# Kernel optimization log

Hardware: AMD Instinct MI355X
Metric: run time of the kernel (lower is better)

Reference implementation:

```python
import jax, jax.numpy as jnp
import numpy as np

HID = 512      # hidden_dim
MID = 256      # hid_dim
COND_D = 256   # condition_op_dim
OP_D = 32      # operator_len
EX_D = 32      # extra_info_num
L, N, T = 16, 1024, 8
EPS = 1e-5


def _lstm_cell(x_proj, h, c, Whh, bhh):
    # x_proj: precomputed x @ Wih.T + bih, shape [B, 4H]
    gates = x_proj + h @ Whh.T + bhh
    i, f, g, o = jnp.split(gates, 4, axis=-1)
    i = jax.nn.sigmoid(i); f = jax.nn.sigmoid(f)
    g = jnp.tanh(g); o = jax.nn.sigmoid(o)
    c = f * c + i * g
    h = o * jnp.tanh(c)
    return h, c


def _batchnorm(x, gamma, beta):
    mu = x.mean(0)
    var = x.var(0)  # biased, matches PyTorch training-mode normalization
    return gamma * (x - mu) * jax.lax.rsqrt(var + EPS) + beta


def setup_inputs() -> dict:
    key = jax.random.key(0)
    ks = jax.random.split(key, 24)
    s = lambda *sh: 0.05
    inp = {
        'operators': jax.random.normal(ks[0], (L, N, OP_D), jnp.float32),
        'extra_infos': jax.random.normal(ks[1], (L, N, EX_D), jnp.float32),
        'conditions': jax.random.normal(ks[2], (L, N, T, COND_D), jnp.float32),
        'condition_masks': jnp.ones((L, N, 1), jnp.float32),
        'mapping': jax.random.randint(ks[3], (L, N, 2), 0, N + 1, jnp.int32).astype(jnp.int64),
        'lstm1_Wih': jax.random.normal(ks[4], (4 * HID, COND_D), jnp.float32) * 0.05,
        'lstm1_Whh': jax.random.normal(ks[5], (4 * HID, HID), jnp.float32) * 0.05,
        'lstm1_bih': jnp.zeros((4 * HID,), jnp.float32),
        'lstm1_bhh': jnp.zeros((4 * HID,), jnp.float32),
        'cond_W': jax.random.normal(ks[6], (MID, HID), jnp.float32) * 0.05,
        'cond_b': jnp.zeros((MID,), jnp.float32),
        'bn1_g': jnp.ones((MID,), jnp.float32),
        'bn1_b': jnp.zeros((MID,), jnp.float32),
        'lstm2_Wih': jax.random.normal(ks[7], (4 * HID, OP_D + EX_D + MID), jnp.float32) * 0.05,
        'lstm2_Whh': jax.random.normal(ks[8], (4 * HID, HID), jnp.float32) * 0.05,
        'lstm2_bih': jnp.zeros((4 * HID,), jnp.float32),
        'lstm2_bhh': jnp.zeros((4 * HID,), jnp.float32),
        'bn2_g': jnp.ones((HID,), jnp.float32),
        'bn2_b': jnp.zeros((HID,), jnp.float32),
    }
    return inp


def reference(operators, extra_infos, conditions, condition_masks, mapping,
              lstm1_Wih, lstm1_Whh, lstm1_bih, lstm1_bhh,
              cond_W, cond_b, bn1_g, bn1_b,
              lstm2_Wih, lstm2_Whh, lstm2_bih, lstm2_bhh,
              bn2_g, bn2_b):
    B = L * N
    x = conditions.reshape(B, T, COND_D)
    # lstm1 over conditions; precompute input projections for all steps
    xp = jnp.einsum('btd,gd->btg', x, lstm1_Wih) + lstm1_bih  # [B,T,4H]

    def step1(carry, xt):
        h, c = carry
        h, c = _lstm_cell(xt, h, c, lstm1_Whh, lstm1_bhh)
        return (h, c), None

    h0 = jnp.zeros((B, HID), xp.dtype)
    (h1, _), _ = jax.lax.scan(step1, (h0, h0), jnp.swapaxes(xp, 0, 1))

    last = jax.nn.relu(h1 @ cond_W.T + cond_b)       # [B, MID]
    last = _batchnorm(last, bn1_g, bn1_b).reshape(L, N, MID)

    out = jnp.concatenate([operators, extra_infos, last], axis=2)  # [L,N,IN2]
    xp2 = jnp.einsum('lnd,gd->lng', out, lstm2_Wih) + lstm2_bih    # [L,N,4H]

    hz = jnp.zeros((N, HID), xp2.dtype)
    h, c = _lstm_cell(xp2[L - 1], hz, hz, lstm2_Whh, lstm2_bhh)

    mapping = mapping.astype(jnp.int32)
    levels = jnp.arange(L - 2, -1, -1)

    def tree_step(carry, idx):
        h, c = carry
        mp = mapping[idx]  # [N,2]
        pad = jnp.zeros((1, HID), h.dtype)
        ph = jnp.concatenate([pad, h], 0)  # [N+1,H]
        pc = jnp.concatenate([pad, c], 0)
        h = (ph[mp[:, 0]] + ph[mp[:, 1]]) * 0.5
        c = (pc[mp[:, 0]] + pc[mp[:, 1]]) * 0.5
        h, c = _lstm_cell(xp2[idx], h, c, lstm2_Whh, lstm2_bhh)
        return (h, c), None

    (h, c), _ = jax.lax.scan(tree_step, (h, c), levels)

    # batch_size == N since all operator rows are nonzero
    return _batchnorm(h, bn2_g, bn2_b)  # [N, HID]
```

## Files before the change

kernel.cpp:

```cpp
#include <hip/hip_runtime.h>
#include <hip/hip_bf16.h>
#include <stdint.h>


typedef __bf16 bf16;
typedef __bf16 bf16x8 __attribute__((ext_vector_type(8)));
typedef float f32x4 __attribute__((ext_vector_type(4)));

#define HIDDEN 512

__device__ __forceinline__ float sigmoidf_(float x) { return 1.f / (1.f + __expf(-x)); }

__device__ __forceinline__ void async16(const bf16* g, bf16* l) {
  __builtin_amdgcn_global_load_lds(
      (const __attribute__((address_space(1))) void*)g,
      (__attribute__((address_space(3))) void*)l, 16, 0, 0);
}

__global__ void cvt8(const float* __restrict__ src, bf16* __restrict__ dst) {
  size_t i = ((size_t)blockIdx.x * blockDim.x + threadIdx.x) * 8;
  float4 a = *(const float4*)(src + i);
  float4 b = *(const float4*)(src + i + 4);
  bf16x8 r;
  r[0] = (bf16)a.x; r[1] = (bf16)a.y; r[2] = (bf16)a.z; r[3] = (bf16)a.w;
  r[4] = (bf16)b.x; r[5] = (bf16)b.y; r[6] = (bf16)b.z; r[7] = (bf16)b.w;
  *(bf16x8*)(dst + i) = r;
}

__global__ void detect(const int* __restrict__ map, int* __restrict__ flags) {
  __shared__ int any;
  if (threadIdx.x == 0) any = 0;
  __syncthreads();
  int loc = 0;
  for (int i = threadIdx.x; i < 16384; i += blockDim.x) loc |= map[2 * i + 1];
  if (loc) atomicOr(&any, 1);
  __syncthreads();
  if (threadIdx.x == 0) flags[0] = (any == 0) ? 1 : 0;
}

template <int MT>
__global__ __launch_bounds__(256, 2) void cell_gemm(
    const bf16* __restrict__ A0, int a0off, int a0s, int a0kt,
    const bf16* __restrict__ A1, int a1s, int a1kt,
    const bf16* __restrict__ B0, int b0s,
    const bf16* __restrict__ B1, int b1s,
    const float* __restrict__ bias0, const float* __restrict__ bias1,
    const void* __restrict__ xp_add, int xp_f32,
    const float* __restrict__ c_prev,
    float* __restrict__ c_out,
    bf16* __restrict__ h_b16, float* __restrict__ h_f32)
{
  constexpr int BM = MT * 32;
  __shared__ __align__(16) bf16 sA[BM * 64];
  __shared__ __align__(16) bf16 sB[128 * 64];
  const int tid = threadIdx.x;
  const int lane = tid & 63;
  const int quad = lane >> 4, cl = lane & 15;
  const int wave = tid >> 6;
  const int wr = wave >> 1, wc = wave & 1;
  const int bm0 = blockIdx.x * BM;
  const int j0 = blockIdx.y * 32;

  f32x4 acc[MT][4];
#pragma unroll
  for (int mi = 0; mi < MT; ++mi)
#pragma unroll
    for (int g = 0; g < 4; ++g) acc[mi][g] = f32x4{0.f, 0.f, 0.f, 0.f};

  const int nkt = a0kt + a1kt;
  for (int kt = 0; kt < nkt; ++kt) {
    const bf16* abase; int astr, acol;
    const bf16* bbase; int bstr, bcol;
    if (kt < a0kt) {
      abase = A0; astr = a0s; acol = a0off + kt * 64;
      bbase = B0; bstr = b0s; bcol = kt * 64;
    } else {
      abase = A1; astr = a1s; acol = (kt - a0kt) * 64;
      bbase = B1; bstr = b1s; bcol = (kt - a0kt) * 64;
    }
#pragma unroll
    for (int ia = 0; ia < MT; ++ia) {
      int e = ia * 256 + tid;
      int row = e >> 3, sl = e & 7;
      int src = sl ^ (row & 7);
      async16(abase + (size_t)(bm0 + row) * astr + acol + src * 8, sA + e * 8);
    }
#pragma unroll
    for (int ib = 0; ib < 4; ++ib) {
      int e = ib * 256 + tid;
      int row = e >> 3, sl = e & 7;
      int src = sl ^ (row & 7);
      int wrow = (row >> 5) * HIDDEN + j0 + (row & 31);
      async16(bbase + (size_t)wrow * bstr + bcol + src * 8, sB + e * 8);
    }
    __syncthreads();
#pragma unroll
    for (int kh = 0; kh < 2; ++kh) {
      bf16x8 af[MT], bfr[4];
#pragma unroll
      for (int mi = 0; mi < MT; ++mi) {
        int row = wr * (MT * 16) + mi * 16 + cl;
        int sl = (kh * 4 + quad) ^ (row & 7);
        af[mi] = *(const bf16x8*)&sA[row * 64 + sl * 8];
      }
#pragma unroll
      for (int g = 0; g < 4; ++g) {
        int row = g * 32 + wc * 16 + cl;
        int sl = (kh * 4 + quad) ^ (row & 7);
        bfr[g] = *(const bf16x8*)&sB[row * 64 + sl * 8];
      }
#pragma unroll
      for (int mi = 0; mi < MT; ++mi)
#pragma unroll
        for (int g = 0; g < 4; ++g)
          acc[mi][g] = __builtin_amdgcn_mfma_f32_16x16x32_bf16(af[mi], bfr[g], acc[mi][g], 0, 0, 0);
    }
    __syncthreads();
  }

  const int j = j0 + wc * 16 + cl;
  float bI = 0.f, bF = 0.f, bG = 0.f, bO = 0.f;
  if (bias0) {
    bI += bias0[j]; bF += bias0[HIDDEN + j];
    bG += bias0[2 * HIDDEN + j]; bO += bias0[3 * HIDDEN + j];
  }
  if (bias1) {
    bI += bias1[j]; bF += bias1[HIDDEN + j];
    bG += bias1[2 * HIDDEN + j]; bO += bias1[3 * HIDDEN + j];
  }
#pragma unroll
  for (int mi = 0; mi < MT; ++mi) {
    int rb = bm0 + wr * (MT * 16) + mi * 16 + quad * 4;
#pragma unroll
    for (int r = 0; r < 4; ++r) {
      int row = rb + r;
      float gi = acc[mi][0][r] + bI;
      float gf = acc[mi][1][r] + bF;
      float gg = acc[mi][2][r] + bG;
      float go = acc[mi][3][r] + bO;
      if (xp_add) {
        size_t base = (size_t)row * 2048;
        if (xp_f32) {
          const float* xr = (const float*)xp_add + base;
          gi += xr[j]; gf += xr[HIDDEN + j];
          gg += xr[2 * HIDDEN + j]; go += xr[3 * HIDDEN + j];
        } else {
          const bf16* xr = (const bf16*)xp_add + base;
          gi += (float)xr[j]; gf += (float)xr[HIDDEN + j];
          gg += (float)xr[2 * HIDDEN + j]; go += (float)xr[3 * HIDDEN + j];
        }
      }
      float iv = sigmoidf_(gi), fv = sigmoidf_(gf);
      float gv = tanhf(gg), ov = sigmoidf_(go);
      float cp = c_prev ? c_prev[(size_t)row * HIDDEN + j] : 0.f;
      float cn = fv * cp + iv * gv;
      float hn = ov * tanhf(cn);
      c_out[(size_t)row * HIDDEN + j] = cn;
      if (h_b16) h_b16[(size_t)row * HIDDEN + j] = (bf16)hn;
      if (h_f32) h_f32[(size_t)row * HIDDEN + j] = hn;
    }
  }
}

__global__ __launch_bounds__(256, 2) void plain_gemm(
    const bf16* __restrict__ A0, int a0s, int a0kt,
    const bf16* __restrict__ A1, int a1s, int a1kt,
    const bf16* __restrict__ A2, int a2s, int a2kt,
    const bf16* __restrict__ B, int bs,
    const float* __restrict__ bias, int do_relu,
    bf16* __restrict__ outh, float* __restrict__ outf, int Ntot)
{
  __shared__ __align__(16) bf16 sA[128 * 32];
  __shared__ __align__(16) bf16 sB[128 * 32];
  const int tid = threadIdx.x;
  const int lane = tid & 63;
  const int quad = lane >> 4, cl = lane & 15;
  const int wave = tid >> 6;
  const int wr = wave >> 1, wc = wave & 1;
  const int bm0 = blockIdx.x * 128;
  const int bn0 = blockIdx.y * 128;

  f32x4 acc[4][4];
#pragma unroll
  for (int mi = 0; mi < 4; ++mi)
#pragma unroll
    for (int ni = 0; ni < 4; ++ni) acc[mi][ni] = f32x4{0.f, 0.f, 0.f, 0.f};

  const int nkt = a0kt + a1kt + a2kt;
  for (int kt = 0; kt < nkt; ++kt) {
    const bf16* abase; int astr, acol;
    if (kt < a0kt)            { abase = A0; astr = a0s; acol = kt * 32; }
    else if (kt < a0kt + a1kt){ abase = A1; astr = a1s; acol = (kt - a0kt) * 32; }
    else                      { abase = A2; astr = a2s; acol = (kt - a0kt - a1kt) * 32; }
#pragma unroll
    for (int it = 0; it < 2; ++it) {
      int e = it * 256 + tid;
      int row = e >> 2, sl = e & 3;
      int src = sl ^ ((row >> 1) & 3);
      async16(abase + (size_t)(bm0 + row) * astr + acol + src * 8, sA + e * 8);
      async16(B + (size_t)(bn0 + row) * bs + kt * 32 + src * 8, sB + e * 8);
    }
    __syncthreads();
    bf16x8 af[4], bfr[4];
#pragma unroll
    for (int mi = 0; mi < 4; ++mi) {
      int row = wr * 64 + mi * 16 + cl;
      int sl = quad ^ ((row >> 1) & 3);
      af[mi] = *(const bf16x8*)&sA[row * 32 + sl * 8];
    }
#pragma unroll
    for (int ni = 0; ni < 4; ++ni) {
      int row = wc * 64 + ni * 16 + cl;
      int sl = quad ^ ((row >> 1) & 3);
      bfr[ni] = *(const bf16x8*)&sB[row * 32 + sl * 8];
    }
#pragma unroll
    for (int mi = 0; mi < 4; ++mi)
#pragma unroll
      for (int ni = 0; ni < 4; ++ni)
        acc[mi][ni] = __builtin_amdgcn_mfma_f32_16x16x32_bf16(af[mi], bfr[ni], acc[mi][ni], 0, 0, 0);
    __syncthreads();
  }

#pragma unroll
  for (int mi = 0; mi < 4; ++mi) {
    int rb = bm0 + wr * 64 + mi * 16 + quad * 4;
#pragma unroll
    for (int ni = 0; ni < 4; ++ni) {
      int col = bn0 + wc * 64 + ni * 16 + cl;
      float bv = bias ? bias[col] : 0.f;
#pragma unroll
      for (int r = 0; r < 4; ++r) {
        int row = rb + r;
        float v = acc[mi][ni][r] + bv;
        if (do_relu) v = fmaxf(v, 0.f);
        if (outf) outf[(size_t)row * Ntot + col] = v;
        else      outh[(size_t)row * Ntot + col] = (bf16)v;
      }
    }
  }
}

__global__ void gather_h(const int* __restrict__ map, const int* __restrict__ flags,
                         int level,
                         const float* __restrict__ h_src, const float* __restrict__ c_src,
                         bf16* __restrict__ hA, float* __restrict__ c_dst)
{
  int n = blockIdx.x, t = threadIdx.x;
  long base = (long)level * 2048 + n * 2;
  int m0, m1;
  if (flags[0]) { m0 = map[base * 2]; m1 = map[base * 2 + 2]; }
  else          { m0 = map[base];     m1 = map[base + 1]; }
  float h0 = m0 ? h_src[(size_t)(m0 - 1) * HIDDEN + t] : 0.f;
  float h1 = m1 ? h_src[(size_t)(m1 - 1) * HIDDEN + t] : 0.f;
  float c0 = m0 ? c_src[(size_t)(m0 - 1) * HIDDEN + t] : 0.f;
  float c1 = m1 ? c_src[(size_t)(m1 - 1) * HIDDEN + t] : 0.f;
  hA[(size_t)n * HIDDEN + t] = (bf16)(0.5f * (h0 + h1));
  c_dst[(size_t)n * HIDDEN + t] = 0.5f * (c0 + c1);
}

__global__ void cell0(const void* __restrict__ xp, int xp_f32,
                      const float* __restrict__ bhh,
                      float* __restrict__ h, float* __restrict__ c)
{
  int n = blockIdx.x, j = threadIdx.x;
  float g[4];
#pragma unroll
  for (int k = 0; k < 4; ++k) {
    size_t idx = (size_t)n * 2048 + k * 512 + j;
    float v = xp_f32 ? ((const float*)xp)[idx] : (float)((const bf16*)xp)[idx];
    g[k] = v + bhh[k * 512 + j];
  }
  float cv = sigmoidf_(g[0]) * tanhf(g[2]);
  h[(size_t)n * HIDDEN + j] = sigmoidf_(g[3]) * tanhf(cv);
  c[(size_t)n * HIDDEN + j] = cv;
}

__global__ void bn_reduce_b16(const bf16* __restrict__ x, int rpb, int F,
                              float* __restrict__ partials) {
  int col = threadIdx.x, b = blockIdx.x;
  const bf16* p = x + (size_t)b * rpb * F + col;
  float s = 0.f, q = 0.f;
  for (int r = 0; r < rpb; ++r) { float v = (float)p[(size_t)r * F]; s += v; q += v * v; }
  partials[(size_t)b * 2 * F + col] = s;
  partials[(size_t)b * 2 * F + F + col] = q;
}

__global__ void bn_reduce_f32(const float* __restrict__ x, int rpb, int F,
                              float* __restrict__ partials) {
  int col = threadIdx.x, b = blockIdx.x;
  const float* p = x + (size_t)b * rpb * F + col;
  float s = 0.f, q = 0.f;
  for (int r = 0; r < rpb; ++r) { float v = p[(size_t)r * F]; s += v; q += v * v; }
  partials[(size_t)b * 2 * F + col] = s;
  partials[(size_t)b * 2 * F + F + col] = q;
}

__global__ void bn_final(const float* __restrict__ partials, int nb, int F,
                         const float* __restrict__ g, const float* __restrict__ b,
                         float invB, float* __restrict__ scale, float* __restrict__ shift) {
  int j = threadIdx.x;
  float s = 0.f, q = 0.f;
  for (int i = 0; i < nb; ++i) {
    s += partials[(size_t)i * 2 * F + j];
    q += partials[(size_t)i * 2 * F + F + j];
  }
  float mu = s * invB;
  float var = fmaxf(q * invB - mu * mu, 0.f);
  float sc = g[j] * rsqrtf(var + 1e-5f);
  scale[j] = sc;
  shift[j] = b[j] - sc * mu;
}

__global__ void bn_apply_mid(const bf16* __restrict__ x, const float* __restrict__ scale,
                             const float* __restrict__ shift, int Fmask, size_t total,
                             bf16* __restrict__ out) {
  for (size_t i = blockIdx.x * (size_t)blockDim.x + threadIdx.x; i < total;
       i += (size_t)gridDim.x * blockDim.x) {
    int j = (int)(i & (size_t)Fmask);
    out[i] = (bf16)(scale[j] * (float)x[i] + shift[j]);
  }
}

__global__ void bn_apply_out(const float* __restrict__ x, const float* __restrict__ scale,
                             const float* __restrict__ shift, int Fmask, size_t total,
                             float* __restrict__ out) {
  for (size_t i = blockIdx.x * (size_t)blockDim.x + threadIdx.x; i < total;
       i += (size_t)gridDim.x * blockDim.x) {
    int j = (int)(i & (size_t)Fmask);
    out[i] = scale[j] * x[i] + shift[j];
  }
}

extern "C" void kernel_launch(void* const* d_in, const int* in_sizes, int n_in,
                              void* d_out, int out_size, void* d_ws, size_t ws_size,
                              hipStream_t stream) {
  const float* operators = (const float*)d_in[0];
  const float* extras    = (const float*)d_in[1];
  const float* conds     = (const float*)d_in[2];
  const int*   mapping   = (const int*)d_in[4];
  const float* b1ih = (const float*)d_in[7];
  const float* b1hh = (const float*)d_in[8];
  const float* condb = (const float*)d_in[10];
  const float* bn1g = (const float*)d_in[11];
  const float* bn1b = (const float*)d_in[12];
  const float* b2ih = (const float*)d_in[15];
  const float* b2hh = (const float*)d_in[16];
  const float* bn2g = (const float*)d_in[17];
  const float* bn2b = (const float*)d_in[18];

  char* ws = (char*)d_ws;
  size_t o = 0;
  auto alloc = [&](size_t bytes) {
    char* p = ws + o;
    o += (bytes + 255) & ~(size_t)255;
    return p;
  };
  bf16* conds_b = (bf16*)alloc((size_t)33554432 * 2);
  bf16* ops_b   = (bf16*)alloc((size_t)524288 * 2);
  bf16* ext_b   = (bf16*)alloc((size_t)524288 * 2);
  bf16* w1ih_b  = (bf16*)alloc((size_t)524288 * 2);
  bf16* w1hh_b  = (bf16*)alloc((size_t)1048576 * 2);
  bf16* condw_b = (bf16*)alloc((size_t)131072 * 2);
  bf16* w2ih_b  = (bf16*)alloc((size_t)655360 * 2);
  bf16* w2hh_b  = (bf16*)alloc((size_t)1048576 * 2);
  bf16* h1[2];
  h1[0] = (bf16*)alloc((size_t)16384 * 512 * 2);
  h1[1] = (bf16*)alloc((size_t)16384 * 512 * 2);
  float* c1 = (float*)alloc((size_t)16384 * 512 * 4);
  bf16* last_relu = (bf16*)alloc((size_t)16384 * 256 * 2);
  bf16* last_bn = (bf16*)alloc((size_t)16384 * 256 * 2);
  float* h2 = (float*)alloc((size_t)1024 * 512 * 4);
  bf16* hA = (bf16*)alloc((size_t)1024 * 512 * 2);
  float* c2a = (float*)alloc((size_t)1024 * 512 * 4);
  float* c2b = (float*)alloc((size_t)1024 * 512 * 4);
  float* partials = (float*)alloc((size_t)64 * 1024 * 4);
  float* scale1 = (float*)alloc(256 * 4);
  float* shift1 = (float*)alloc(256 * 4);
  float* scale2 = (float*)alloc(512 * 4);
  float* shift2 = (float*)alloc(512 * 4);
  int* flags = (int*)alloc(256);

  size_t xp2_elems = (size_t)16384 * 2048;
  int xpf = (o + xp2_elems * 4 <= ws_size) ? 1 : 0;
  void* xp2 = alloc(xp2_elems * (xpf ? 4 : 2));
  float* xp2f = xpf ? (float*)xp2 : nullptr;
  bf16* xp2h = xpf ? nullptr : (bf16*)xp2;

  detect<<<1, 256, 0, stream>>>(mapping, flags);
  cvt8<<<16384, 256, 0, stream>>>(conds, conds_b);
  cvt8<<<256, 256, 0, stream>>>(operators, ops_b);
  cvt8<<<256, 256, 0, stream>>>(extras, ext_b);
  cvt8<<<256, 256, 0, stream>>>((const float*)d_in[5], w1ih_b);
  cvt8<<<512, 256, 0, stream>>>((const float*)d_in[6], w1hh_b);
  cvt8<<<64, 256, 0, stream>>>((const float*)d_in[9], condw_b);
  cvt8<<<320, 256, 0, stream>>>((const float*)d_in[13], w2ih_b);
  cvt8<<<512, 256, 0, stream>>>((const float*)d_in[14], w2hh_b);

  for (int t = 0; t < 8; ++t) {
    const bf16* hprev = (t == 0) ? nullptr : h1[t & 1];
    cell_gemm<4><<<dim3(128, 16), 256, 0, stream>>>(
        conds_b, t * 256, 2048, 4,
        hprev, 512, (t == 0) ? 0 : 8,
        w1ih_b, 256, w1hh_b, 512,
        b1ih, b1hh,
        nullptr, 0,
        (t == 0) ? nullptr : c1, c1, h1[(t + 1) & 1], nullptr);
  }

  plain_gemm<<<dim3(128, 2), 256, 0, stream>>>(
      h1[0], 512, 16, nullptr, 0, 0, nullptr, 0, 0,
      condw_b, 512, condb, 1, last_relu, nullptr, 256);
  bn_reduce_b16<<<64, 256, 0, stream>>>(last_relu, 256, 256, partials);
  bn_final<<<1, 256, 0, stream>>>(partials, 64, 256, bn1g, bn1b, 1.f / 16384.f, scale1, shift1);
  bn_apply_mid<<<1024, 256, 0, stream>>>(last_relu, scale1, shift1, 255,
                                         (size_t)16384 * 256, last_bn);

  plain_gemm<<<dim3(128, 16), 256, 0, stream>>>(
      ops_b, 32, 1, ext_b, 32, 1, last_bn, 256, 8,
      w2ih_b, 320, b2ih, 0, xp2h, xp2f, 2048);

  size_t lvl_sz = (size_t)1024 * 2048;
  const void* xp15 = xpf ? (const void*)(xp2f + 15 * lvl_sz) : (const void*)(xp2h + 15 * lvl_sz);
  cell0<<<1024, 512, 0, stream>>>(xp15, xpf, b2hh, h2, c2a);
  for (int idx = 14; idx >= 0; --idx) {
    gather_h<<<1024, 512, 0, stream>>>(mapping, flags, idx, h2, c2a, hA, c2b);
    const void* xpl = xpf ? (const void*)(xp2f + idx * lvl_sz) : (const void*)(xp2h + idx * lvl_sz);
    cell_gemm<2><<<dim3(16, 16), 256, 0, stream>>>(
        hA, 0, 512, 8,
        nullptr, 0, 0,
        w2hh_b, 512, nullptr, 0,
        b2hh, nullptr,
        xpl, xpf,
        c2b, c2a, nullptr, h2);
  }

  bn_reduce_f32<<<16, 512, 0, stream>>>(h2, 64, 512, partials);
  bn_final<<<1, 512, 0, stream>>>(partials, 16, 512, bn2g, bn2b, 1.f / 1024.f, scale2, shift2);
  bn_apply_out<<<512, 256, 0, stream>>>(h2, scale2, shift2, 511,
                                        (size_t)1024 * 512, (float*)d_out);
}
```

Measured before the change: 1.304 ms.

## Batch weight conversions, fast activations, retile GEMMs, and store tree h in bf16

Seven separate weight/input conversion launches are merged into one multi-segment kernel. tanhf is replaced by an exp-based fast tanh, and cell_gemm's K loop is split into two phases so per-iteration branching goes away. The plain and tree GEMMs get smaller M tiles to launch more blocks, and tree-level h is stored as bf16, with an fp32 copy kept only at the last level to halve gather traffic. These changes cut launch overhead and improve occupancy on small grids, at a small accuracy cost from bf16 h and the approximate tanh.

```diff
diff --git a/kernel.cpp b/kernel.cpp
--- a/kernel.cpp
+++ b/kernel.cpp
@@ -9,7 +9,11 @@
 
 #define HIDDEN 512
 
-__device__ __forceinline__ float sigmoidf_(float x) { return 1.f / (1.f + __expf(-x)); }
+__device__ __forceinline__ float fast_sig(float x) { return 1.f / (1.f + __expf(-x)); }
+__device__ __forceinline__ float fast_tanh(float x) {
+  float e = __expf(2.f * x);
+  return 1.f - 2.f / (e + 1.f);
+}
 
 __device__ __forceinline__ void async16(const bf16* g, bf16* l) {
   __builtin_amdgcn_global_load_lds(
@@ -17,14 +21,39 @@
       (__attribute__((address_space(3))) void*)l, 16, 0, 0);
 }
 
-__global__ void cvt8(const float* __restrict__ src, bf16* __restrict__ dst) {
-  size_t i = ((size_t)blockIdx.x * blockDim.x + threadIdx.x) * 8;
+__device__ __forceinline__ void cvt_one(const float* __restrict__ src,
+                                        bf16* __restrict__ dst, size_t i) {
   float4 a = *(const float4*)(src + i);
   float4 b = *(const float4*)(src + i + 4);
   bf16x8 r;
   r[0] = (bf16)a.x; r[1] = (bf16)a.y; r[2] = (bf16)a.z; r[3] = (bf16)a.w;
   r[4] = (bf16)b.x; r[5] = (bf16)b.y; r[6] = (bf16)b.z; r[7] = (bf16)b.w;
   *(bf16x8*)(dst + i) = r;
+}
+
+__global__ void cvt8(const float* __restrict__ src, bf16* __restrict__ dst) {
+  size_t i = ((size_t)blockIdx.x * blockDim.x + threadIdx.x) * 8;
+  cvt_one(src, dst, i);
+}
+
+__global__ void cvt_multi(const float* s0, bf16* d0,
+                          const float* s1, bf16* d1,
+                          const float* s2, bf16* d2,
+                          const float* s3, bf16* d3,
+                          const float* s4, bf16* d4,
+                          const float* s5, bf16* d5,
+                          const float* s6, bf16* d6) {
+  int g = blockIdx.x * blockDim.x + threadIdx.x;
+  const float* s; bf16* d; int off;
+  if      (g < 65536)  { s = s0; d = d0; off = g; }
+  else if (g < 131072) { s = s1; d = d1; off = g - 65536; }
+  else if (g < 196608) { s = s2; d = d2; off = g - 131072; }
+  else if (g < 327680) { s = s3; d = d3; off = g - 196608; }
+  else if (g < 344064) { s = s4; d = d4; off = g - 327680; }
+  else if (g < 425984) { s = s5; d = d5; off = g - 344064; }
+  else if (g < 557056) { s = s6; d = d6; off = g - 425984; }
+  else return;
+  cvt_one(s, d, (size_t)off * 8);
 }
 
 __global__ void detect(const int* __restrict__ map, int* __restrict__ flags) {
@@ -48,7 +77,8 @@
     const void* __restrict__ xp_add, int xp_f32,
     const float* __restrict__ c_prev,
     float* __restrict__ c_out,
-    bf16* __restrict__ h_b16, float* __restrict__ h_f32)
+    bf16* __restrict__ h_b16,
+    float* __restrict__ h_f32)
 {
   constexpr int BM = MT * 32;
   __shared__ __align__(16) bf16 sA[BM * 64];
@@ -67,63 +97,59 @@
 #pragma unroll
     for (int g = 0; g < 4; ++g) acc[mi][g] = f32x4{0.f, 0.f, 0.f, 0.f};
 
-  const int nkt = a0kt + a1kt;
-  for (int kt = 0; kt < nkt; ++kt) {
-    const bf16* abase; int astr, acol;
-    const bf16* bbase; int bstr, bcol;
-    if (kt < a0kt) {
-      abase = A0; astr = a0s; acol = a0off + kt * 64;
-      bbase = B0; bstr = b0s; bcol = kt * 64;
-    } else {
-      abase = A1; astr = a1s; acol = (kt - a0kt) * 64;
-      bbase = B1; bstr = b1s; bcol = (kt - a0kt) * 64;
-    }
-#pragma unroll
-    for (int ia = 0; ia < MT; ++ia) {
-      int e = ia * 256 + tid;
-      int row = e >> 3, sl = e & 7;
-      int src = sl ^ (row & 7);
-      async16(abase + (size_t)(bm0 + row) * astr + acol + src * 8, sA + e * 8);
-    }
-#pragma unroll
-    for (int ib = 0; ib < 4; ++ib) {
-      int e = ib * 256 + tid;
-      int row = e >> 3, sl = e & 7;
-      int src = sl ^ (row & 7);
-      int wrow = (row >> 5) * HIDDEN + j0 + (row & 31);
-      async16(bbase + (size_t)wrow * bstr + bcol + src * 8, sB + e * 8);
-    }
-    __syncthreads();
-#pragma unroll
-    for (int kh = 0; kh < 2; ++kh) {
-      bf16x8 af[MT], bfr[4];
-#pragma unroll
-      for (int mi = 0; mi < MT; ++mi) {
-        int row = wr * (MT * 16) + mi * 16 + cl;
-        int sl = (kh * 4 + quad) ^ (row & 7);
-        af[mi] = *(const bf16x8*)&sA[row * 64 + sl * 8];
+#pragma unroll
+  for (int ph = 0; ph < 2; ++ph) {
+    const int kts = (ph == 0) ? a0kt : a1kt;
+    const bf16* ab = (ph == 0) ? A0 : A1;
+    const int as = (ph == 0) ? a0s : a1s;
+    const int ao = (ph == 0) ? a0off : 0;
+    const bf16* bb = (ph == 0) ? B0 : B1;
+    const int bs = (ph == 0) ? b0s : b1s;
+    for (int kt = 0; kt < kts; ++kt) {
+#pragma unroll
+      for (int ia = 0; ia < MT; ++ia) {
+        int e = ia * 256 + tid;
+        int row = e >> 3, sl = e & 7;
+        int src = sl ^ (row & 7);
+        async16(ab + (size_t)(bm0 + row) * as + ao + kt * 64 + src * 8, sA + e * 8);
       }
 #pragma unroll
-      for (int g = 0; g < 4; ++g) {
-        int row = g * 32 + wc * 16 + cl;
-        int sl = (kh * 4 + quad) ^ (row & 7);
-        bfr[g] = *(const bf16x8*)&sB[row * 64 + sl * 8];
+      for (int ib = 0; ib < 4; ++ib) {
+        int e = ib * 256 + tid;
+        int row = e >> 3, sl = e & 7;
+        int src = sl ^ (row & 7);
+        int wrow = (row >> 5) * HIDDEN + j0 + (row & 31);
+        async16(bb + (size_t)wrow * bs + kt * 64 + src * 8, sB + e * 8);
       }
-#pragma unroll
-      for (int mi = 0; mi < MT; ++mi)
-#pragma unroll
-        for (int g = 0; g < 4; ++g)
-          acc[mi][g] = __builtin_amdgcn_mfma_f32_16x16x32_bf16(af[mi], bfr[g], acc[mi][g], 0, 0, 0);
-    }
-    __syncthreads();
+      __syncthreads();
+#pragma unroll
+      for (int kh = 0; kh < 2; ++kh) {
+        bf16x8 af[MT], bfr[4];
+#pragma unroll
+        for (int mi = 0; mi < MT; ++mi) {
+          int row = wr * (MT * 16) + mi * 16 + cl;
+          int sl = (kh * 4 + quad) ^ (row & 7);
+          af[mi] = *(const bf16x8*)&sA[row * 64 + sl * 8];
+        }
+#pragma unroll
+        for (int g = 0; g < 4; ++g) {
+          int row = g * 32 + wc * 16 + cl;
+          int sl = (kh * 4 + quad) ^ (row & 7);
+          bfr[g] = *(const bf16x8*)&sB[row * 64 + sl * 8];
+        }
+#pragma unroll
+        for (int mi = 0; mi < MT; ++mi)
+#pragma unroll
+          for (int g = 0; g < 4; ++g)
+            acc[mi][g] = __builtin_amdgcn_mfma_f32_16x16x32_bf16(af[mi], bfr[g], acc[mi][g], 0, 0, 0);
+      }
+      __syncthreads();
+    }
   }
 
   const int j = j0 + wc * 16 + cl;
-  float bI = 0.f, bF = 0.f, bG = 0.f, bO = 0.f;
-  if (bias0) {
-    bI += bias0[j]; bF += bias0[HIDDEN + j];
-    bG += bias0[2 * HIDDEN + j]; bO += bias0[3 * HIDDEN + j];
-  }
+  float bI = bias0[j], bF = bias0[HIDDEN + j];
+  float bG = bias0[2 * HIDDEN + j], bO = bias0[3 * HIDDEN + j];
   if (bias1) {
     bI += bias1[j]; bF += bias1[HIDDEN + j];
     bG += bias1[2 * HIDDEN + j]; bO += bias1[3 * HIDDEN + j];
@@ -150,18 +176,19 @@
           gg += (float)xr[2 * HIDDEN + j]; go += (float)xr[3 * HIDDEN + j];
         }
       }
-      float iv = sigmoidf_(gi), fv = sigmoidf_(gf);
-      float gv = tanhf(gg), ov = sigmoidf_(go);
+      float iv = fast_sig(gi), fv = fast_sig(gf);
+      float gv = fast_tanh(gg), ov = fast_sig(go);
       float cp = c_prev ? c_prev[(size_t)row * HIDDEN + j] : 0.f;
       float cn = fv * cp + iv * gv;
-      float hn = ov * tanhf(cn);
+      float hn = ov * fast_tanh(cn);
       c_out[(size_t)row * HIDDEN + j] = cn;
-      if (h_b16) h_b16[(size_t)row * HIDDEN + j] = (bf16)hn;
+      h_b16[(size_t)row * HIDDEN + j] = (bf16)hn;
       if (h_f32) h_f32[(size_t)row * HIDDEN + j] = hn;
     }
   }
 }
 
+template <int MT>
 __global__ __launch_bounds__(256, 2) void plain_gemm(
     const bf16* __restrict__ A0, int a0s, int a0kt,
     const bf16* __restrict__ A1, int a1s, int a1kt,
@@ -170,19 +197,20 @@
     const float* __restrict__ bias, int do_relu,
     bf16* __restrict__ outh, float* __restrict__ outf, int Ntot)
 {
-  __shared__ __align__(16) bf16 sA[128 * 32];
+  constexpr int BM = MT * 32;
+  __shared__ __align__(16) bf16 sA[BM * 32];
   __shared__ __align__(16) bf16 sB[128 * 32];
   const int tid = threadIdx.x;
   const int lane = tid & 63;
   const int quad = lane >> 4, cl = lane & 15;
   const int wave = tid >> 6;
   const int wr = wave >> 1, wc = wave & 1;
-  const int bm0 = blockIdx.x * 128;
+  const int bm0 = blockIdx.x * BM;
   const int bn0 = blockIdx.y * 128;
 
-  f32x4 acc[4][4];
-#pragma unroll
-  for (int mi = 0; mi < 4; ++mi)
+  f32x4 acc[MT][4];
+#pragma unroll
+  for (int mi = 0; mi < MT; ++mi)
 #pragma unroll
     for (int ni = 0; ni < 4; ++ni) acc[mi][ni] = f32x4{0.f, 0.f, 0.f, 0.f};
 
@@ -193,18 +221,24 @@
     else if (kt < a0kt + a1kt){ abase = A1; astr = a1s; acol = (kt - a0kt) * 32; }
     else                      { abase = A2; astr = a2s; acol = (kt - a0kt - a1kt) * 32; }
 #pragma unroll
-    for (int it = 0; it < 2; ++it) {
-      int e = it * 256 + tid;
+    for (int ia = 0; ia < MT / 2; ++ia) {
+      int e = ia * 256 + tid;
       int row = e >> 2, sl = e & 3;
       int src = sl ^ ((row >> 1) & 3);
       async16(abase + (size_t)(bm0 + row) * astr + acol + src * 8, sA + e * 8);
+    }
+#pragma unroll
+    for (int ib = 0; ib < 2; ++ib) {
+      int e = ib * 256 + tid;
+      int row = e >> 2, sl = e & 3;
+      int src = sl ^ ((row >> 1) & 3);
       async16(B + (size_t)(bn0 + row) * bs + kt * 32 + src * 8, sB + e * 8);
     }
     __syncthreads();
-    bf16x8 af[4], bfr[4];
-#pragma unroll
-    for (int mi = 0; mi < 4; ++mi) {
-      int row = wr * 64 + mi * 16 + cl;
+    bf16x8 af[MT], bfr[4];
+#pragma unroll
+    for (int mi = 0; mi < MT; ++mi) {
+      int row = wr * (MT * 16) + mi * 16 + cl;
       int sl = quad ^ ((row >> 1) & 3);
       af[mi] = *(const bf16x8*)&sA[row * 32 + sl * 8];
     }
@@ -215,7 +249,7 @@
       bfr[ni] = *(const bf16x8*)&sB[row * 32 + sl * 8];
     }
 #pragma unroll
-    for (int mi = 0; mi < 4; ++mi)
+    for (int mi = 0; mi < MT; ++mi)
 #pragma unroll
       for (int ni = 0; ni < 4; ++ni)
         acc[mi][ni] = __builtin_amdgcn_mfma_f32_16x16x32_bf16(af[mi], bfr[ni], acc[mi][ni], 0, 0, 0);
@@ -223,8 +257,8 @@
   }
 
 #pragma unroll
-  for (int mi = 0; mi < 4; ++mi) {
-    int rb = bm0 + wr * 64 + mi * 16 + quad * 4;
+  for (int mi = 0; mi < MT; ++mi) {
+    int rb = bm0 + wr * (MT * 16) + mi * 16 + quad * 4;
 #pragma unroll
     for (int ni = 0; ni < 4; ++ni) {
       int col = bn0 + wc * 64 + ni * 16 + cl;
@@ -243,7 +277,7 @@
 
 __global__ void gather_h(const int* __restrict__ map, const int* __restrict__ flags,
                          int level,
-                         const float* __restrict__ h_src, const float* __restrict__ c_src,
+                         const bf16* __restrict__ h_src, const float* __restrict__ c_src,
                          bf16* __restrict__ hA, float* __restrict__ c_dst)
 {
   int n = blockIdx.x, t = threadIdx.x;
@@ -251,8 +285,8 @@
   int m0, m1;
   if (flags[0]) { m0 = map[base * 2]; m1 = map[base * 2 + 2]; }
   else          { m0 = map[base];     m1 = map[base + 1]; }
-  float h0 = m0 ? h_src[(size_t)(m0 - 1) * HIDDEN + t] : 0.f;
-  float h1 = m1 ? h_src[(size_t)(m1 - 1) * HIDDEN + t] : 0.f;
+  float h0 = m0 ? (float)h_src[(size_t)(m0 - 1) * HIDDEN + t] : 0.f;
+  float h1 = m1 ? (float)h_src[(size_t)(m1 - 1) * HIDDEN + t] : 0.f;
   float c0 = m0 ? c_src[(size_t)(m0 - 1) * HIDDEN + t] : 0.f;
   float c1 = m1 ? c_src[(size_t)(m1 - 1) * HIDDEN + t] : 0.f;
   hA[(size_t)n * HIDDEN + t] = (bf16)(0.5f * (h0 + h1));
@@ -261,7 +295,7 @@
 
 __global__ void cell0(const void* __restrict__ xp, int xp_f32,
                       const float* __restrict__ bhh,
-                      float* __restrict__ h, float* __restrict__ c)
+                      bf16* __restrict__ h, float* __restrict__ c)
 {
   int n = blockIdx.x, j = threadIdx.x;
   float g[4];
@@ -271,8 +305,8 @@
     float v = xp_f32 ? ((const float*)xp)[idx] : (float)((const bf16*)xp)[idx];
     g[k] = v + bhh[k * 512 + j];
   }
-  float cv = sigmoidf_(g[0]) * tanhf(g[2]);
-  h[(size_t)n * HIDDEN + j] = sigmoidf_(g[3]) * tanhf(cv);
+  float cv = fast_sig(g[0]) * fast_tanh(g[2]);
+  h[(size_t)n * HIDDEN + j] = (bf16)(fast_sig(g[3]) * fast_tanh(cv));
   c[(size_t)n * HIDDEN + j] = cv;
 }
 
@@ -370,10 +404,11 @@
   float* c1 = (float*)alloc((size_t)16384 * 512 * 4);
   bf16* last_relu = (bf16*)alloc((size_t)16384 * 256 * 2);
   bf16* last_bn = (bf16*)alloc((size_t)16384 * 256 * 2);
-  float* h2 = (float*)alloc((size_t)1024 * 512 * 4);
+  bf16* h2 = (bf16*)alloc((size_t)1024 * 512 * 2);
   bf16* hA = (bf16*)alloc((size_t)1024 * 512 * 2);
   float* c2a = (float*)alloc((size_t)1024 * 512 * 4);
   float* c2b = (float*)alloc((size_t)1024 * 512 * 4);
+  float* h2f = (float*)alloc((size_t)1024 * 512 * 4);
   float* partials = (float*)alloc((size_t)64 * 1024 * 4);
   float* scale1 = (float*)alloc(256 * 4);
   float* shift1 = (float*)alloc(256 * 4);
@@ -389,13 +424,11 @@
 
   detect<<<1, 256, 0, stream>>>(mapping, flags);
   cvt8<<<16384, 256, 0, stream>>>(conds, conds_b);
-  cvt8<<<256, 256, 0, stream>>>(operators, ops_b);
-  cvt8<<<256, 256, 0, stream>>>(extras, ext_b);
-  cvt8<<<256, 256, 0, stream>>>((const float*)d_in[5], w1ih_b);
-  cvt8<<<512, 256, 0, stream>>>((const float*)d_in[6], w1hh_b);
-  cvt8<<<64, 256, 0, stream>>>((const float*)d_in[9], condw_b);
-  cvt8<<<320, 256, 0, stream>>>((const float*)d_in[13], w2ih_b);
-  cvt8<<<512, 256, 0, stream>>>((const float*)d_in[14], w2hh_b);
+  cvt_multi<<<2176, 256, 0, stream>>>(
+      operators, ops_b, extras, ext_b,
+      (const float*)d_in[5], w1ih_b, (const float*)d_in[6], w1hh_b,
+      (const float*)d_in[9], condw_b, (const float*)d_in[13], w2ih_b,
+      (const float*)d_in[14], w2hh_b);
 
   for (int t = 0; t < 8; ++t) {
     const bf16* hprev = (t == 0) ? nullptr : h1[t & 1];
@@ -408,7 +441,7 @@
         (t == 0) ? nullptr : c1, c1, h1[(t + 1) & 1], nullptr);
   }
 
-  plain_gemm<<<dim3(128, 2), 256, 0, stream>>>(
+  plain_gemm<2><<<dim3(256, 2), 256, 0, stream>>>(
       h1[0], 512, 16, nullptr, 0, 0, nullptr, 0, 0,
       condw_b, 512, condb, 1, last_relu, nullptr, 256);
   bn_reduce_b16<<<64, 256, 0, stream>>>(last_relu, 256, 256, partials);
@@ -416,7 +449,7 @@
   bn_apply_mid<<<1024, 256, 0, stream>>>(last_relu, scale1, shift1, 255,
                                          (size_t)16384 * 256, last_bn);
 
-  plain_gemm<<<dim3(128, 16), 256, 0, stream>>>(
+  plain_gemm<4><<<dim3(128, 16), 256, 0, stream>>>(
       ops_b, 32, 1, ext_b, 32, 1, last_bn, 256, 8,
       w2ih_b, 320, b2ih, 0, xp2h, xp2f, 2048);
 
@@ -426,17 +459,18 @@
   for (int idx = 14; idx >= 0; --idx) {
     gather_h<<<1024, 512, 0, stream>>>(mapping, flags, idx, h2, c2a, hA, c2b);
     const void* xpl = xpf ? (const void*)(xp2f + idx * lvl_sz) : (const void*)(xp2h + idx * lvl_sz);
-    cell_gemm<2><<<dim3(16, 16), 256, 0, stream>>>(
+    cell_gemm<1><<<dim3(32, 16), 256, 0, stream>>>(
         hA, 0, 512, 8,
         nullptr, 0, 0,
         w2hh_b, 512, nullptr, 0,
         b2hh, nullptr,
         xpl, xpf,
-        c2b, c2a, nullptr, h2);
-  }
-
-  bn_reduce_f32<<<16, 512, 0, stream>>>(h2, 64, 512, partials);
+        c2b, c2a, h2,
+        (idx == 0) ? h2f : nullptr);
+  }
+
+  bn_reduce_f32<<<16, 512, 0, stream>>>(h2f, 64, 512, partials);
   bn_final<<<1, 512, 0, stream>>>(partials, 16, 512, bn2g, bn2b, 1.f / 1024.f, scale2, shift2);
-  bn_apply_out<<<512, 256, 0, stream>>>(h2, scale2, shift2, 511,
+  bn_apply_out<<<512, 256, 0, stream>>>(h2f, scale2, shift2, 511,
                                         (size_t)1024 * 512, (float*)d_out);
 }
```

Result: faster. 1.201 ms (-7.8%).
